# Kernel optimization log

Hardware: AMD Instinct MI355X
Metric: run time of the kernel (lower is better)

Reference implementation:

```python
import jax, jax.numpy as jnp
import numpy as np


def _lstm_dir(x, Wih, Whh, bih, bhh, reverse):
    """Single-direction LSTM. x: [T,B,Cin]; PyTorch gate order i,f,g,o."""
    T, B, _ = x.shape
    H = Whh.shape[1]
    # Precompute input-to-hidden GEMM for all timesteps at once: [T,B,4H]
    xg = jnp.einsum('tbc,gc->tbg', x, Wih) + (bih + bhh)

    def step(carry, xt):
        h, c = carry
        gates = xt + h @ Whh.T  # [B,4H]
        i, f, g, o = jnp.split(gates, 4, axis=-1)
        i = jax.nn.sigmoid(i)
        f = jax.nn.sigmoid(f)
        g = jnp.tanh(g)
        o = jax.nn.sigmoid(o)
        c = f * c + i * g
        h = o * jnp.tanh(c)
        return (h, c), h

    init = (jnp.zeros((B, H), x.dtype), jnp.zeros((B, H), x.dtype))
    _, hs = jax.lax.scan(step, init, xg, reverse=reverse)
    return hs  # [T,B,H], time-aligned with x for both directions


def _bilstm_layer(x, Wih_f, Whh_f, bih_f, bhh_f, Wih_b, Whh_b, bih_b, bhh_b):
    hf = _lstm_dir(x, Wih_f, Whh_f, bih_f, bhh_f, reverse=False)
    hb = _lstm_dir(x, Wih_b, Whh_b, bih_b, bhh_b, reverse=True)
    return jnp.concatenate([hf, hb], axis=-1)  # [T,B,2H]


def setup_inputs() -> dict:
    key = jax.random.key(0)
    ks = jax.random.split(key, 18)
    T, B, C, H = 160, 256, 512, 256
    G = 4 * H  # 1024
    s = 0.05  # small init to keep gates in the linear-ish regime
    inp = {"x": jax.random.normal(ks[0], (T, B, C), jnp.float32)}
    names = []
    for l, cin in ((0, C), (1, 2 * H)):
        for sfx in ("", "_reverse"):
            names.append((f"weight_ih_l{l}{sfx}", (G, cin)))
            names.append((f"weight_hh_l{l}{sfx}", (G, H)))
            names.append((f"bias_ih_l{l}{sfx}", (G,)))
            names.append((f"bias_hh_l{l}{sfx}", (G,)))
    for i, (nm, shp) in enumerate(names):
        inp[nm] = jax.random.normal(ks[i + 1], shp, jnp.float32) * s
    return inp


def reference(x,
              weight_ih_l0, weight_hh_l0, bias_ih_l0, bias_hh_l0,
              weight_ih_l0_reverse, weight_hh_l0_reverse, bias_ih_l0_reverse, bias_hh_l0_reverse,
              weight_ih_l1, weight_hh_l1, bias_ih_l1, bias_hh_l1,
              weight_ih_l1_reverse, weight_hh_l1_reverse, bias_ih_l1_reverse, bias_hh_l1_reverse):
    h0 = _bilstm_layer(x,
                       weight_ih_l0, weight_hh_l0, bias_ih_l0, bias_hh_l0,
                       weight_ih_l0_reverse, weight_hh_l0_reverse, bias_ih_l0_reverse, bias_hh_l0_reverse)
    h1 = _bilstm_layer(h0,
                       weight_ih_l1, weight_hh_l1, bias_ih_l1, bias_hh_l1,
                       weight_ih_l1_reverse, weight_hh_l1_reverse, bias_ih_l1_reverse, bias_hh_l1_reverse)
    return h1  # [T, B, 2H]
```

## Files before the change

kernel.cpp:

```cpp
#include <hip/hip_runtime.h>
#include <stdint.h>

typedef __attribute__((ext_vector_type(8))) short bf16x8;
typedef __attribute__((ext_vector_type(4))) float f32x4;

__device__ __forceinline__ float bf2f(unsigned short u) {
    union { unsigned int u32; float f; } v; v.u32 = ((unsigned int)u) << 16; return v.f;
}
__device__ __forceinline__ unsigned short f2bf(float f) {
    union { float f; unsigned int u32; } v; v.f = f;
    unsigned int r = v.u32 + 0x7FFFu + ((v.u32 >> 16) & 1u);
    return (unsigned short)(r >> 16);
}
__device__ __forceinline__ float sigm(float x) { return 1.f / (1.f + __expf(-x)); }
__device__ __forceinline__ float tanh_fast(float x) {
    float ax = fabsf(x);
    float e = __expf(-2.f * ax);
    float t = (1.f - e) / (1.f + e);
    return copysignf(t, x);
}

__global__ void f2bf_kernel(const float* __restrict__ src, unsigned short* __restrict__ dst, int n4) {
    int i = blockIdx.x * blockDim.x + threadIdx.x;
    if (i >= n4) return;
    float4 v = ((const float4*)src)[i];
    ushort4 o;
    o.x = f2bf(v.x); o.y = f2bf(v.y); o.z = f2bf(v.z); o.w = f2bf(v.w);
    ((ushort4*)dst)[i] = o;
}

__global__ void bias_comb_kernel(const float* __restrict__ bif, const float* __restrict__ bhf,
                                 const float* __restrict__ bir, const float* __restrict__ bhr,
                                 float* __restrict__ out) {
    int n = blockIdx.x * blockDim.x + threadIdx.x;
    if (n >= 2048) return;
    out[n] = (n < 1024) ? (bif[n] + bhf[n]) : (bir[n - 1024] + bhr[n - 1024]);
}

__global__ __launch_bounds__(256, 2) void gemm_bt_bias(
    const unsigned short* __restrict__ A, const unsigned short* __restrict__ B,
    const float* __restrict__ bias, unsigned short* __restrict__ C,
    int M, int N, int K) {
    const int bn0 = blockIdx.x * 128;
    const int bm0 = blockIdx.y * 128;
    const int tid = threadIdx.x;
    const int wave = tid >> 6, lane = tid & 63;
    const int ln15 = lane & 15, quad = lane >> 4;
    const int wr = wave >> 1, wc = wave & 1;

    __shared__ __align__(16) unsigned short At[128 * 72];
    __shared__ __align__(16) unsigned short Bt[128 * 72];

    f32x4 acc[4][4] = {};

    for (int ko = 0; ko < K; ko += 64) {
#pragma unroll
        for (int i = 0; i < 4; ++i) {
            int chunk = tid + i * 256;
            int row = chunk >> 3, cc = chunk & 7;
            *(bf16x8*)&At[row * 72 + cc * 8] = *(const bf16x8*)&A[(size_t)(bm0 + row) * K + ko + cc * 8];
            *(bf16x8*)&Bt[row * 72 + cc * 8] = *(const bf16x8*)&B[(size_t)(bn0 + row) * K + ko + cc * 8];
        }
        __syncthreads();
#pragma unroll
        for (int kk = 0; kk < 2; ++kk) {
            bf16x8 a[4], b[4];
#pragma unroll
            for (int f = 0; f < 4; ++f) {
                a[f] = *(const bf16x8*)&At[(wr * 64 + f * 16 + ln15) * 72 + kk * 32 + quad * 8];
                b[f] = *(const bf16x8*)&Bt[(wc * 64 + f * 16 + ln15) * 72 + kk * 32 + quad * 8];
            }
#pragma unroll
            for (int fi = 0; fi < 4; ++fi)
#pragma unroll
                for (int fj = 0; fj < 4; ++fj)
                    acc[fi][fj] = __builtin_amdgcn_mfma_f32_16x16x32_bf16(a[fi], b[fj], acc[fi][fj], 0, 0, 0);
        }
        __syncthreads();
    }
#pragma unroll
    for (int fi = 0; fi < 4; ++fi) {
        int row = bm0 + wr * 64 + fi * 16 + quad * 4;
#pragma unroll
        for (int fj = 0; fj < 4; ++fj) {
            int col = bn0 + wc * 64 + fj * 16 + ln15;
            float bv = bias[col];
#pragma unroll
            for (int r = 0; r < 4; ++r)
                C[(size_t)(row + r) * N + col] = f2bf(acc[fi][fj][r] + bv);
        }
    }
}

__global__ __launch_bounds__(256, 1) void lstm_scan4(
    const unsigned short* __restrict__ xg,
    const unsigned short* __restrict__ whh_f,
    const unsigned short* __restrict__ whh_r,
    unsigned short* __restrict__ out_bf,
    float* __restrict__ out_f,
    unsigned short* __restrict__ hexg)
{
    const int gid = blockIdx.x & 31;
    const int cg = blockIdx.x >> 5;
    const int dir = gid & 1, bg = gid >> 1;
    const int m0 = bg * 16;
    const int tid = threadIdx.x;
    const int wave = tid >> 6, lane = tid & 63;
    const int ln15 = lane & 15, quad = lane >> 4;
    const unsigned short* __restrict__ whh = dir ? whh_r : whh_f;

    __shared__ float gbuf[2][16 * 260];

    bf16x8 Bfr[32];
#pragma unroll
    for (int kb = 0; kb < 8; ++kb)
#pragma unroll
        for (int nt = 0; nt < 4; ++nt)
            Bfr[kb * 4 + nt] = *(const bf16x8*)&whh[
                (size_t)(wave * 256 + cg * 64 + nt * 16 + ln15) * 256 + kb * 32 + quad * 8];

    const int cm = tid >> 4, cj = tid & 15;
    float c[4] = {0.f, 0.f, 0.f, 0.f};

    unsigned long long* hex64 = (unsigned long long*)hexg;
    const unsigned long long SENT = ~0ull;

    for (int tt = 0; tt < 160; ++tt) {
        const int t = dir ? (159 - tt) : tt;

        f32x4 acc[4];
        {
            const unsigned short* xr = xg + (size_t)(t * 256 + m0 + quad * 4) * 2048
                                          + dir * 1024 + wave * 256 + cg * 64 + ln15;
#pragma unroll
            for (int nt = 0; nt < 4; ++nt)
#pragma unroll
                for (int r = 0; r < 4; ++r)
                    acc[nt][r] = bf2f(xr[(size_t)r * 2048 + nt * 16]);
        }

        const int slot_r = (tt + 7) & 7;
        unsigned long long* hsrc = hex64 + ((size_t)(slot_r * 2 + dir) * 16 + bg) * 1024
                                 + ln15 * 64 + quad * 2;
        unsigned long long w[16];
        {
            int lim = 1 << 20;
            for (;;) {
                bool ok = true;
#pragma unroll
                for (int kb = 0; kb < 8; ++kb) {
                    w[kb * 2]     = __hip_atomic_load(hsrc + kb * 8,     __ATOMIC_RELAXED, __HIP_MEMORY_SCOPE_AGENT);
                    w[kb * 2 + 1] = __hip_atomic_load(hsrc + kb * 8 + 1, __ATOMIC_RELAXED, __HIP_MEMORY_SCOPE_AGENT);
                }
#pragma unroll
                for (int i = 0; i < 16; ++i) ok &= (w[i] != SENT);
                if (ok || !--lim) break;
                __builtin_amdgcn_s_sleep(2);
            }
        }

        {
            const int slot_p = (tt + 6) & 7;
            unsigned long long* pp = hex64 + ((size_t)(slot_p * 2 + dir) * 16 + bg) * 1024
                                   + cm * 64 + cg * 16 + cj;
            __hip_atomic_store(pp, SENT, __ATOMIC_RELAXED, __HIP_MEMORY_SCOPE_AGENT);
        }

        bf16x8 af[8];
#pragma unroll
        for (int kb = 0; kb < 8; ++kb) {
            union { unsigned long long u[2]; bf16x8 v; } tm;
            tm.u[0] = w[kb * 2]; tm.u[1] = w[kb * 2 + 1];
            af[kb] = tm.v;
        }

#pragma unroll
        for (int kb = 0; kb < 8; ++kb)
#pragma unroll
            for (int nt = 0; nt < 4; ++nt)
                acc[nt] = __builtin_amdgcn_mfma_f32_16x16x32_bf16(af[kb], Bfr[kb * 4 + nt], acc[nt], 0, 0, 0);

        const int par = tt & 1;
#pragma unroll
        for (int nt = 0; nt < 4; ++nt)
#pragma unroll
            for (int r = 0; r < 4; ++r) {
                float v = acc[nt][r];
                v = (wave == 2) ? tanh_fast(v) : sigm(v);
                gbuf[par][(quad * 4 + r) * 260 + wave * 64 + nt * 16 + ln15] = v;
            }
        __syncthreads();

        const int slot_w = tt & 7;
        unsigned long long* hdst = hex64 + ((size_t)(slot_w * 2 + dir) * 16 + bg) * 1024;
        const float* gb = gbuf[par] + cm * 260;
        float hv[4];
#pragma unroll
        for (int p = 0; p < 4; ++p) {
            int lj = cj * 4 + p;
            float iv = gb[lj];
            float fv = gb[64 + lj];
            float gv = gb[128 + lj];
            float ov = gb[192 + lj];
            float cn = fv * c[p] + iv * gv;
            c[p] = cn;
            hv[p] = ov * tanh_fast(cn);
        }
        unsigned long long pk = (unsigned long long)f2bf(hv[0])
                              | ((unsigned long long)f2bf(hv[1]) << 16)
                              | ((unsigned long long)f2bf(hv[2]) << 32)
                              | ((unsigned long long)f2bf(hv[3]) << 48);
        __hip_atomic_store(hdst + cm * 64 + cg * 16 + cj, pk,
                           __ATOMIC_RELAXED, __HIP_MEMORY_SCOPE_AGENT);

        size_t obase = (size_t)(t * 256 + m0 + cm) * 512 + dir * 256 + cg * 64 + cj * 4;
        if (out_f) {
            float4 o4; o4.x = hv[0]; o4.y = hv[1]; o4.z = hv[2]; o4.w = hv[3];
            *(float4*)&out_f[obase] = o4;
        } else {
            ushort4 o4;
            o4.x = f2bf(hv[0]); o4.y = f2bf(hv[1]); o4.z = f2bf(hv[2]); o4.w = f2bf(hv[3]);
            *(ushort4*)&out_bf[obase] = o4;
        }
    }
}

extern "C" void kernel_launch(void* const* d_in, const int* in_sizes, int n_in,
                              void* d_out, int out_size, void* d_ws, size_t ws_size,
                              hipStream_t stream) {
    const float* x = (const float*)d_in[0];
    float* out = (float*)d_out;
    char* ws = (char*)d_ws;

    unsigned short* xbf   = (unsigned short*)(ws + 0);
    unsigned short* wcat0 = (unsigned short*)(ws + 41943040LL);
    unsigned short* wcat1 = (unsigned short*)(ws + 44040192LL);
    unsigned short* whh0f = (unsigned short*)(ws + 46137344LL);
    unsigned short* whh0r = whh0f + 262144;
    unsigned short* whh1f = whh0f + 524288;
    unsigned short* whh1r = whh0f + 786432;
    float* bias0          = (float*)(ws + 48234496LL);
    float* bias1          = (float*)(ws + 48242688LL);
    unsigned short* xgbuf = (unsigned short*)(ws + 48250880LL);
    unsigned short* hexg  = wcat0;
    unsigned short* h0b   = xbf;

    f2bf_kernel<<<20480, 256, 0, stream>>>(x, xbf, 5242880);
    f2bf_kernel<<<512, 256, 0, stream>>>((const float*)d_in[1], wcat0, 131072);
    f2bf_kernel<<<512, 256, 0, stream>>>((const float*)d_in[5], wcat0 + 524288, 131072);
    f2bf_kernel<<<512, 256, 0, stream>>>((const float*)d_in[9], wcat1, 131072);
    f2bf_kernel<<<512, 256, 0, stream>>>((const float*)d_in[13], wcat1 + 524288, 131072);
    f2bf_kernel<<<256, 256, 0, stream>>>((const float*)d_in[2], whh0f, 65536);
    f2bf_kernel<<<256, 256, 0, stream>>>((const float*)d_in[6], whh0r, 65536);
    f2bf_kernel<<<256, 256, 0, stream>>>((const float*)d_in[10], whh1f, 65536);
    f2bf_kernel<<<256, 256, 0, stream>>>((const float*)d_in[14], whh1r, 65536);
    bias_comb_kernel<<<8, 256, 0, stream>>>((const float*)d_in[3], (const float*)d_in[4],
                                            (const float*)d_in[7], (const float*)d_in[8], bias0);
    bias_comb_kernel<<<8, 256, 0, stream>>>((const float*)d_in[11], (const float*)d_in[12],
                                            (const float*)d_in[15], (const float*)d_in[16], bias1);

    dim3 gg(16, 320);
    gemm_bt_bias<<<gg, 256, 0, stream>>>(xbf, wcat0, bias0, xgbuf, 40960, 2048, 512);
    hipMemsetAsync(hexg, 0xFF, 2097152, stream);
    hipMemsetAsync((char*)hexg + 7 * 262144, 0, 262144, stream);
    lstm_scan4<<<128, 256, 0, stream>>>(xgbuf, whh0f, whh0r, h0b, nullptr, hexg);
    gemm_bt_bias<<<gg, 256, 0, stream>>>(h0b, wcat1, bias1, xgbuf, 40960, 2048, 512);
    hipMemsetAsync(hexg, 0xFF, 2097152, stream);
    hipMemsetAsync((char*)hexg + 7 * 262144, 0, 262144, stream);
    lstm_scan4<<<128, 256, 0, stream>>>(xgbuf, whh1f, whh1r, nullptr, out, hexg);
}
```

Measured before the change: 1.743 ms.

## Restructure LSTM scan: per-wave gate ownership, sc0 polling, x prefetch

Reorganizes the recurrent scan so each wave computes all four gates for its own hidden columns. This removes the LDS gate buffer and one of the two block barriers per timestep. The next timestep's input-gate values are prefetched into registers, and lane shuffles repack h into the exchange layout. A startup handshake checks whether plain sc0 loads and stores are coherent across the blocks. If they are, inline-asm dwordx4 polling without sleep replaces the agent-scope atomics, otherwise the atomic path is kept. The non-atomic path depends on cache-coherence behaviour, and the handshake adds startup overhead.

```diff
diff --git a/kernel.cpp b/kernel.cpp
--- a/kernel.cpp
+++ b/kernel.cpp
@@ -3,6 +3,7 @@
 
 typedef __attribute__((ext_vector_type(8))) short bf16x8;
 typedef __attribute__((ext_vector_type(4))) float f32x4;
+typedef __attribute__((ext_vector_type(2))) unsigned long long u64x2;
 
 __device__ __forceinline__ float bf2f(unsigned short u) {
     union { unsigned int u32; float f; } v; v.u32 = ((unsigned int)u) << 16; return v.f;
@@ -92,137 +93,240 @@
     }
 }
 
-__global__ __launch_bounds__(256, 1) void lstm_scan4(
+__device__ __forceinline__ void st1_sc0(unsigned long long* p, unsigned long long v) {
+    asm volatile("global_store_dwordx2 %0, %1, off sc0" :: "v"(p), "v"(v) : "memory");
+}
+__device__ __forceinline__ unsigned long long ld1_sc0(const unsigned long long* p) {
+    unsigned long long v;
+    asm volatile("global_load_dwordx2 %0, %1, off sc0\n\ts_waitcnt vmcnt(0)"
+                 : "=v"(v) : "v"(p) : "memory");
+    return v;
+}
+
+template<bool FAST>
+__device__ void scan_loop(const unsigned short* __restrict__ xg,
+                          const unsigned short* __restrict__ whh,
+                          unsigned short* __restrict__ out_bf,
+                          float* __restrict__ out_f,
+                          unsigned long long* hex64, int dir, int bg, int cg)
+{
+    const int tid = threadIdx.x;
+    const int wave = tid >> 6, lane = tid & 63;
+    const int ln15 = lane & 15, quad = lane >> 4;
+    const int m0 = bg * 16;
+    const int rowr = quad * 4 + (ln15 & 3);
+    const int colg = cg * 16 + wave * 4 + (ln15 >> 2);
+    const unsigned long long SENT = ~0ull;
+    const unsigned long long M16 = 0x0000FFFF0000FFFFull;
+
+    bf16x8 Bfr[32];
+#pragma unroll
+    for (int kb = 0; kb < 8; ++kb)
+#pragma unroll
+        for (int g = 0; g < 4; ++g)
+            Bfr[kb * 4 + g] = *(const bf16x8*)&whh[
+                (size_t)(g * 256 + cg * 64 + wave * 16 + ln15) * 256 + kb * 32 + quad * 8];
+
+    float c[4] = {0.f, 0.f, 0.f, 0.f};
+    const unsigned short* xbase = xg + (size_t)(m0 + quad * 4) * 2048
+                                     + dir * 1024 + cg * 64 + wave * 16 + ln15;
+
+    unsigned short xvA[16], xvB[16];
+    {
+        const int t0 = dir ? 159 : 0;
+        const unsigned short* xr = xbase + (size_t)t0 * 256 * 2048;
+#pragma unroll
+        for (int g = 0; g < 4; ++g)
+#pragma unroll
+            for (int r = 0; r < 4; ++r)
+                xvA[g * 4 + r] = xr[(size_t)r * 2048 + g * 256];
+    }
+
+    auto step = [&](int tt, unsigned short (&xu)[16], unsigned short (&xp)[16]) {
+        const int t = dir ? (159 - tt) : tt;
+
+        const int slot_r = (tt + 7) & 7;
+        unsigned long long* hsrc = hex64 + ((size_t)(slot_r * 2 + dir) * 16 + bg) * 1024
+                                 + ln15 * 64 + quad * 2;
+        unsigned long long w[16];
+        if (FAST) {
+            u64x2 wv[8];
+            int lim = 1 << 16;
+            for (;;) {
+#define RL(I, OFF) asm volatile("global_load_dwordx4 %0, %1, off offset:" OFF " sc0" : "=v"(wv[I]) : "v"(hsrc))
+                RL(0, "0");  RL(1, "64");  RL(2, "128"); RL(3, "192");
+                RL(4, "256"); RL(5, "320"); RL(6, "384"); RL(7, "448");
+#undef RL
+                asm volatile("s_waitcnt vmcnt(0)" ::: "memory");
+                __builtin_amdgcn_sched_barrier(0);
+                bool ok = true;
+#pragma unroll
+                for (int i = 0; i < 8; ++i) ok &= (wv[i][0] != SENT) & (wv[i][1] != SENT);
+                if (ok || !--lim) break;
+            }
+#pragma unroll
+            for (int i = 0; i < 8; ++i) { w[i * 2] = wv[i][0]; w[i * 2 + 1] = wv[i][1]; }
+        } else {
+            int lim = 1 << 17;
+            for (;;) {
+#pragma unroll
+                for (int kb = 0; kb < 8; ++kb) {
+                    w[kb * 2]     = __hip_atomic_load(hsrc + kb * 8,     __ATOMIC_RELAXED, __HIP_MEMORY_SCOPE_AGENT);
+                    w[kb * 2 + 1] = __hip_atomic_load(hsrc + kb * 8 + 1, __ATOMIC_RELAXED, __HIP_MEMORY_SCOPE_AGENT);
+                }
+                bool ok = true;
+#pragma unroll
+                for (int i = 0; i < 16; ++i) ok &= (w[i] != SENT);
+                if (ok || !--lim) break;
+                __builtin_amdgcn_s_sleep(2);
+            }
+        }
+
+        __syncthreads();
+
+        {
+            const int ttn = (tt < 159) ? tt + 1 : tt;
+            const int tn = dir ? (159 - ttn) : ttn;
+            const unsigned short* xr = xbase + (size_t)tn * 256 * 2048;
+#pragma unroll
+            for (int g = 0; g < 4; ++g)
+#pragma unroll
+                for (int r = 0; r < 4; ++r)
+                    xp[g * 4 + r] = xr[(size_t)r * 2048 + g * 256];
+        }
+
+        bf16x8 af[8];
+#pragma unroll
+        for (int kb = 0; kb < 8; ++kb) {
+            union { unsigned long long u[2]; bf16x8 v; } tm;
+            tm.u[0] = w[kb * 2]; tm.u[1] = w[kb * 2 + 1];
+            af[kb] = tm.v;
+        }
+        f32x4 acc[4] = {};
+#pragma unroll
+        for (int kb = 0; kb < 8; ++kb)
+#pragma unroll
+            for (int g = 0; g < 4; ++g)
+                acc[g] = __builtin_amdgcn_mfma_f32_16x16x32_bf16(af[kb], Bfr[kb * 4 + g], acc[g], 0, 0, 0);
+
+        float hv[4];
+#pragma unroll
+        for (int r = 0; r < 4; ++r) {
+            float iv = sigm(acc[0][r] + bf2f(xu[0 + r]));
+            float fv = sigm(acc[1][r] + bf2f(xu[4 + r]));
+            float gv = tanh_fast(acc[2][r] + bf2f(xu[8 + r]));
+            float ov = sigm(acc[3][r] + bf2f(xu[12 + r]));
+            float cn = fv * c[r] + iv * gv;
+            c[r] = cn;
+            hv[r] = ov * tanh_fast(cn);
+        }
+
+        unsigned long long P = (unsigned long long)f2bf(hv[0])
+                             | ((unsigned long long)f2bf(hv[1]) << 16)
+                             | ((unsigned long long)f2bf(hv[2]) << 32)
+                             | ((unsigned long long)f2bf(hv[3]) << 48);
+        unsigned long long X = __shfl_xor(P, 2);
+        unsigned long long Nn = (ln15 & 2) ? ((X >> 32) | (P & 0xFFFFFFFF00000000ull))
+                                           : ((P & 0x00000000FFFFFFFFull) | (X << 32));
+        unsigned long long Y = __shfl_xor(Nn, 1);
+        unsigned long long Q = (ln15 & 1) ? (((Y >> 16) & M16) | (((Nn >> 16) & M16) << 16))
+                                          : ((Nn & M16) | ((Y & M16) << 16));
+
+        unsigned long long* hdst = hex64 + ((size_t)((tt & 7) * 2 + dir) * 16 + bg) * 1024
+                                 + rowr * 64 + colg;
+        if (FAST) st1_sc0(hdst, Q);
+        else __hip_atomic_store(hdst, Q, __ATOMIC_RELAXED, __HIP_MEMORY_SCOPE_AGENT);
+
+        {
+            const int slot_p = (tt + 6) & 7;
+            unsigned long long* pp = hex64 + ((size_t)(slot_p * 2 + dir) * 16 + bg) * 1024
+                                   + rowr * 64 + colg;
+            if (FAST) st1_sc0(pp, SENT);
+            else __hip_atomic_store(pp, SENT, __ATOMIC_RELAXED, __HIP_MEMORY_SCOPE_AGENT);
+        }
+
+        if (out_f) {
+            size_t ob = (size_t)(t * 256 + m0 + quad * 4) * 512 + dir * 256
+                      + cg * 64 + wave * 16 + ln15;
+#pragma unroll
+            for (int r = 0; r < 4; ++r) out_f[ob + (size_t)r * 512] = hv[r];
+        } else {
+            size_t ob = (size_t)(t * 256 + m0 + rowr) * 512 + dir * 256
+                      + cg * 64 + wave * 16 + (ln15 >> 2) * 4;
+            *(unsigned long long*)&out_bf[ob] = Q;
+        }
+    };
+
+    for (int tt = 0; tt < 160; tt += 2) { step(tt, xvA, xvB); step(tt + 1, xvB, xvA); }
+}
+
+__global__ __launch_bounds__(256, 1) void lstm_scan7(
     const unsigned short* __restrict__ xg,
     const unsigned short* __restrict__ whh_f,
     const unsigned short* __restrict__ whh_r,
     unsigned short* __restrict__ out_bf,
     float* __restrict__ out_f,
-    unsigned short* __restrict__ hexg)
+    unsigned short* __restrict__ hexg,
+    unsigned long long* __restrict__ sync)
 {
     const int gid = blockIdx.x & 31;
     const int cg = blockIdx.x >> 5;
     const int dir = gid & 1, bg = gid >> 1;
-    const int m0 = bg * 16;
-    const int tid = threadIdx.x;
-    const int wave = tid >> 6, lane = tid & 63;
-    const int ln15 = lane & 15, quad = lane >> 4;
     const unsigned short* __restrict__ whh = dir ? whh_r : whh_f;
-
-    __shared__ float gbuf[2][16 * 260];
-
-    bf16x8 Bfr[32];
-#pragma unroll
-    for (int kb = 0; kb < 8; ++kb)
-#pragma unroll
-        for (int nt = 0; nt < 4; ++nt)
-            Bfr[kb * 4 + nt] = *(const bf16x8*)&whh[
-                (size_t)(wave * 256 + cg * 64 + nt * 16 + ln15) * 256 + kb * 32 + quad * 8];
-
-    const int cm = tid >> 4, cj = tid & 15;
-    float c[4] = {0.f, 0.f, 0.f, 0.f};
-
     unsigned long long* hex64 = (unsigned long long*)hexg;
-    const unsigned long long SENT = ~0ull;
-
-    for (int tt = 0; tt < 160; ++tt) {
-        const int t = dir ? (159 - tt) : tt;
-
-        f32x4 acc[4];
-        {
-            const unsigned short* xr = xg + (size_t)(t * 256 + m0 + quad * 4) * 2048
-                                          + dir * 1024 + wave * 256 + cg * 64 + ln15;
-#pragma unroll
-            for (int nt = 0; nt < 4; ++nt)
-#pragma unroll
-                for (int r = 0; r < 4; ++r)
-                    acc[nt][r] = bf2f(xr[(size_t)r * 2048 + nt * 16]);
-        }
-
-        const int slot_r = (tt + 7) & 7;
-        unsigned long long* hsrc = hex64 + ((size_t)(slot_r * 2 + dir) * 16 + bg) * 1024
-                                 + ln15 * 64 + quad * 2;
-        unsigned long long w[16];
+
+    __shared__ int s_fast;
+    if (threadIdx.x == 0) {
+        unsigned long long* can = sync;
+        int* SA = (int*)(sync + 128);
+        int* RR = SA + 128;
+        const int b = blockIdx.x;
+        const unsigned long long M1 = 0x1111111111111111ull, M2 = 0x2222222222222222ull;
+        int ok = 1;
+        st1_sc0(&can[b], M1);
+        {
+            int lim = 1 << 14;
+            for (int p = 0; p < 4; ++p) {
+                unsigned long long v;
+                do { v = ld1_sc0(&can[gid + 32 * p]); } while (v != M1 && --lim > 0);
+                if (v != M1) ok = 0;
+            }
+        }
+        __hip_atomic_store(&SA[b], 1, __ATOMIC_RELAXED, __HIP_MEMORY_SCOPE_AGENT);
         {
             int lim = 1 << 20;
-            for (;;) {
-                bool ok = true;
-#pragma unroll
-                for (int kb = 0; kb < 8; ++kb) {
-                    w[kb * 2]     = __hip_atomic_load(hsrc + kb * 8,     __ATOMIC_RELAXED, __HIP_MEMORY_SCOPE_AGENT);
-                    w[kb * 2 + 1] = __hip_atomic_load(hsrc + kb * 8 + 1, __ATOMIC_RELAXED, __HIP_MEMORY_SCOPE_AGENT);
-                }
-#pragma unroll
-                for (int i = 0; i < 16; ++i) ok &= (w[i] != SENT);
-                if (ok || !--lim) break;
-                __builtin_amdgcn_s_sleep(2);
-            }
-        }
-
-        {
-            const int slot_p = (tt + 6) & 7;
-            unsigned long long* pp = hex64 + ((size_t)(slot_p * 2 + dir) * 16 + bg) * 1024
-                                   + cm * 64 + cg * 16 + cj;
-            __hip_atomic_store(pp, SENT, __ATOMIC_RELAXED, __HIP_MEMORY_SCOPE_AGENT);
-        }
-
-        bf16x8 af[8];
-#pragma unroll
-        for (int kb = 0; kb < 8; ++kb) {
-            union { unsigned long long u[2]; bf16x8 v; } tm;
-            tm.u[0] = w[kb * 2]; tm.u[1] = w[kb * 2 + 1];
-            af[kb] = tm.v;
-        }
-
-#pragma unroll
-        for (int kb = 0; kb < 8; ++kb)
-#pragma unroll
-            for (int nt = 0; nt < 4; ++nt)
-                acc[nt] = __builtin_amdgcn_mfma_f32_16x16x32_bf16(af[kb], Bfr[kb * 4 + nt], acc[nt], 0, 0, 0);
-
-        const int par = tt & 1;
-#pragma unroll
-        for (int nt = 0; nt < 4; ++nt)
-#pragma unroll
-            for (int r = 0; r < 4; ++r) {
-                float v = acc[nt][r];
-                v = (wave == 2) ? tanh_fast(v) : sigm(v);
-                gbuf[par][(quad * 4 + r) * 260 + wave * 64 + nt * 16 + ln15] = v;
-            }
-        __syncthreads();
-
-        const int slot_w = tt & 7;
-        unsigned long long* hdst = hex64 + ((size_t)(slot_w * 2 + dir) * 16 + bg) * 1024;
-        const float* gb = gbuf[par] + cm * 260;
-        float hv[4];
-#pragma unroll
-        for (int p = 0; p < 4; ++p) {
-            int lj = cj * 4 + p;
-            float iv = gb[lj];
-            float fv = gb[64 + lj];
-            float gv = gb[128 + lj];
-            float ov = gb[192 + lj];
-            float cn = fv * c[p] + iv * gv;
-            c[p] = cn;
-            hv[p] = ov * tanh_fast(cn);
-        }
-        unsigned long long pk = (unsigned long long)f2bf(hv[0])
-                              | ((unsigned long long)f2bf(hv[1]) << 16)
-                              | ((unsigned long long)f2bf(hv[2]) << 32)
-                              | ((unsigned long long)f2bf(hv[3]) << 48);
-        __hip_atomic_store(hdst + cm * 64 + cg * 16 + cj, pk,
-                           __ATOMIC_RELAXED, __HIP_MEMORY_SCOPE_AGENT);
-
-        size_t obase = (size_t)(t * 256 + m0 + cm) * 512 + dir * 256 + cg * 64 + cj * 4;
-        if (out_f) {
-            float4 o4; o4.x = hv[0]; o4.y = hv[1]; o4.z = hv[2]; o4.w = hv[3];
-            *(float4*)&out_f[obase] = o4;
-        } else {
-            ushort4 o4;
-            o4.x = f2bf(hv[0]); o4.y = f2bf(hv[1]); o4.z = f2bf(hv[2]); o4.w = f2bf(hv[3]);
-            *(ushort4*)&out_bf[obase] = o4;
-        }
+            for (int p = 0; p < 4; ++p) {
+                int v;
+                do { v = __hip_atomic_load(&SA[gid + 32 * p], __ATOMIC_RELAXED, __HIP_MEMORY_SCOPE_AGENT); }
+                while (v != 1 && --lim > 0);
+                if (v != 1) ok = 0;
+            }
+        }
+        st1_sc0(&can[b], M2);
+        {
+            int lim = 1 << 14;
+            for (int p = 0; p < 4; ++p) {
+                unsigned long long v;
+                do { v = ld1_sc0(&can[gid + 32 * p]); } while (v != M2 && --lim > 0);
+                if (v != M2) ok = 0;
+            }
+        }
+        __hip_atomic_store(&RR[b], ok, __ATOMIC_RELAXED, __HIP_MEMORY_SCOPE_AGENT);
+        int fast = 1;
+        {
+            int lim = 1 << 20;
+            for (int p = 0; p < 4; ++p) {
+                int v;
+                do { v = __hip_atomic_load(&RR[gid + 32 * p], __ATOMIC_RELAXED, __HIP_MEMORY_SCOPE_AGENT); }
+                while (v == -1 && --lim > 0);
+                fast &= (v == 1);
+            }
+        }
+        s_fast = fast;
     }
+    __syncthreads();
+    if (s_fast) scan_loop<true>(xg, whh, out_bf, out_f, hex64, dir, bg, cg);
+    else        scan_loop<false>(xg, whh, out_bf, out_f, hex64, dir, bg, cg);
 }
 
 extern "C" void kernel_launch(void* const* d_in, const int* in_sizes, int n_in,
@@ -242,6 +346,7 @@
     float* bias0          = (float*)(ws + 48234496LL);
     float* bias1          = (float*)(ws + 48242688LL);
     unsigned short* xgbuf = (unsigned short*)(ws + 48250880LL);
+    unsigned long long* syncb = (unsigned long long*)(ws + 216023040LL);
     unsigned short* hexg  = wcat0;
     unsigned short* h0b   = xbf;
 
@@ -263,9 +368,11 @@
     gemm_bt_bias<<<gg, 256, 0, stream>>>(xbf, wcat0, bias0, xgbuf, 40960, 2048, 512);
     hipMemsetAsync(hexg, 0xFF, 2097152, stream);
     hipMemsetAsync((char*)hexg + 7 * 262144, 0, 262144, stream);
-    lstm_scan4<<<128, 256, 0, stream>>>(xgbuf, whh0f, whh0r, h0b, nullptr, hexg);
+    hipMemsetAsync(syncb, 0xFF, 2048, stream);
+    lstm_scan7<<<128, 256, 0, stream>>>(xgbuf, whh0f, whh0r, h0b, nullptr, hexg, syncb);
     gemm_bt_bias<<<gg, 256, 0, stream>>>(h0b, wcat1, bias1, xgbuf, 40960, 2048, 512);
     hipMemsetAsync(hexg, 0xFF, 2097152, stream);
     hipMemsetAsync((char*)hexg + 7 * 262144, 0, 262144, stream);
-    lstm_scan4<<<128, 256, 0, stream>>>(xgbuf, whh1f, whh1r, nullptr, out, hexg);
-}
+    hipMemsetAsync(syncb, 0xFF, 2048, stream);
+    lstm_scan7<<<128, 256, 0, stream>>>(xgbuf, whh1f, whh1r, nullptr, out, hexg, syncb);
+}
```

Result: slower. 5.392 ms (+209.3%).

## Restructure LSTM scan with per-block flags, in-register gates, and x prefetch

Applied to the files above, without the earlier changes.

Replaces the per-element sentinel polling on the hidden-state exchange buffer with per-timestep block flags that one thread spins on, followed by a block barrier. Remaps the recurrent weights so each wave holds all four gates for its columns, so the gate nonlinearities and cell update run in registers without the shared-memory gate buffer. Packs h with lane shuffles, double-buffers h in two slots instead of eight, and prefetches next-step xg values. Adds an extra __syncthreads per step plus a flag store/poll, and relies on relaxed atomics for ordering between the h stores and the flag.

```diff
diff --git a/kernel.cpp b/kernel.cpp
--- a/kernel.cpp
+++ b/kernel.cpp
@@ -92,13 +92,14 @@
     }
 }
 
-__global__ __launch_bounds__(256, 1) void lstm_scan4(
+__global__ __launch_bounds__(256, 1) void lstm_scan8(
     const unsigned short* __restrict__ xg,
     const unsigned short* __restrict__ whh_f,
     const unsigned short* __restrict__ whh_r,
     unsigned short* __restrict__ out_bf,
     float* __restrict__ out_f,
-    unsigned short* __restrict__ hexg)
+    unsigned short* __restrict__ hexg,
+    int* __restrict__ flags)
 {
     const int gid = blockIdx.x & 31;
     const int cg = blockIdx.x >> 5;
@@ -107,63 +108,73 @@
     const int tid = threadIdx.x;
     const int wave = tid >> 6, lane = tid & 63;
     const int ln15 = lane & 15, quad = lane >> 4;
+    const int rowr = quad * 4 + (ln15 & 3);
+    const int colg = cg * 16 + wave * 4 + (ln15 >> 2);
     const unsigned short* __restrict__ whh = dir ? whh_r : whh_f;
-
-    __shared__ float gbuf[2][16 * 260];
+    const unsigned long long M16 = 0x0000FFFF0000FFFFull;
+    unsigned long long* hex64 = (unsigned long long*)hexg;
+    int* fgrp = flags + gid * 160 * 4;
 
     bf16x8 Bfr[32];
 #pragma unroll
     for (int kb = 0; kb < 8; ++kb)
 #pragma unroll
-        for (int nt = 0; nt < 4; ++nt)
-            Bfr[kb * 4 + nt] = *(const bf16x8*)&whh[
-                (size_t)(wave * 256 + cg * 64 + nt * 16 + ln15) * 256 + kb * 32 + quad * 8];
-
-    const int cm = tid >> 4, cj = tid & 15;
+        for (int g = 0; g < 4; ++g)
+            Bfr[kb * 4 + g] = *(const bf16x8*)&whh[
+                (size_t)(g * 256 + cg * 64 + wave * 16 + ln15) * 256 + kb * 32 + quad * 8];
+
     float c[4] = {0.f, 0.f, 0.f, 0.f};
-
-    unsigned long long* hex64 = (unsigned long long*)hexg;
-    const unsigned long long SENT = ~0ull;
-
-    for (int tt = 0; tt < 160; ++tt) {
+    const unsigned short* xbase = xg + (size_t)(m0 + quad * 4) * 2048
+                                     + dir * 1024 + cg * 64 + wave * 16 + ln15;
+
+    unsigned short xvA[16], xvB[16];
+    {
+        const int t0 = dir ? 159 : 0;
+        const unsigned short* xr = xbase + (size_t)t0 * 256 * 2048;
+#pragma unroll
+        for (int g = 0; g < 4; ++g)
+#pragma unroll
+            for (int r = 0; r < 4; ++r)
+                xvA[g * 4 + r] = xr[(size_t)r * 2048 + g * 256];
+    }
+
+    auto step = [&](int tt, unsigned short (&xu)[16], unsigned short (&xp)[16]) {
         const int t = dir ? (159 - tt) : tt;
 
-        f32x4 acc[4];
-        {
-            const unsigned short* xr = xg + (size_t)(t * 256 + m0 + quad * 4) * 2048
-                                          + dir * 1024 + wave * 256 + cg * 64 + ln15;
-#pragma unroll
-            for (int nt = 0; nt < 4; ++nt)
-#pragma unroll
-                for (int r = 0; r < 4; ++r)
-                    acc[nt][r] = bf2f(xr[(size_t)r * 2048 + nt * 16]);
-        }
-
-        const int slot_r = (tt + 7) & 7;
+        if (tt > 0) {
+            if (tid == 0) {
+                const int* fp = fgrp + (tt - 1) * 4;
+                int lim = 1 << 22;
+                for (;;) {
+                    int a0 = __hip_atomic_load(fp + 0, __ATOMIC_RELAXED, __HIP_MEMORY_SCOPE_AGENT);
+                    int a1 = __hip_atomic_load(fp + 1, __ATOMIC_RELAXED, __HIP_MEMORY_SCOPE_AGENT);
+                    int a2 = __hip_atomic_load(fp + 2, __ATOMIC_RELAXED, __HIP_MEMORY_SCOPE_AGENT);
+                    int a3 = __hip_atomic_load(fp + 3, __ATOMIC_RELAXED, __HIP_MEMORY_SCOPE_AGENT);
+                    if ((a0 & a1 & a2 & a3) || !--lim) break;
+                }
+            }
+            __syncthreads();
+        }
+
+        const int slot_r = (tt + 1) & 1;
         unsigned long long* hsrc = hex64 + ((size_t)(slot_r * 2 + dir) * 16 + bg) * 1024
                                  + ln15 * 64 + quad * 2;
         unsigned long long w[16];
+#pragma unroll
+        for (int kb = 0; kb < 8; ++kb) {
+            w[kb * 2]     = __hip_atomic_load(hsrc + kb * 8,     __ATOMIC_RELAXED, __HIP_MEMORY_SCOPE_AGENT);
+            w[kb * 2 + 1] = __hip_atomic_load(hsrc + kb * 8 + 1, __ATOMIC_RELAXED, __HIP_MEMORY_SCOPE_AGENT);
+        }
+
         {
-            int lim = 1 << 20;
-            for (;;) {
-                bool ok = true;
-#pragma unroll
-                for (int kb = 0; kb < 8; ++kb) {
-                    w[kb * 2]     = __hip_atomic_load(hsrc + kb * 8,     __ATOMIC_RELAXED, __HIP_MEMORY_SCOPE_AGENT);
-                    w[kb * 2 + 1] = __hip_atomic_load(hsrc + kb * 8 + 1, __ATOMIC_RELAXED, __HIP_MEMORY_SCOPE_AGENT);
-                }
-#pragma unroll
-                for (int i = 0; i < 16; ++i) ok &= (w[i] != SENT);
-                if (ok || !--lim) break;
-                __builtin_amdgcn_s_sleep(2);
-            }
-        }
-
-        {
-            const int slot_p = (tt + 6) & 7;
-            unsigned long long* pp = hex64 + ((size_t)(slot_p * 2 + dir) * 16 + bg) * 1024
-                                   + cm * 64 + cg * 16 + cj;
-            __hip_atomic_store(pp, SENT, __ATOMIC_RELAXED, __HIP_MEMORY_SCOPE_AGENT);
+            const int ttn = (tt < 159) ? tt + 1 : tt;
+            const int tn = dir ? (159 - ttn) : ttn;
+            const unsigned short* xr = xbase + (size_t)tn * 256 * 2048;
+#pragma unroll
+            for (int g = 0; g < 4; ++g)
+#pragma unroll
+                for (int r = 0; r < 4; ++r)
+                    xp[g * 4 + r] = xr[(size_t)r * 2048 + g * 256];
         }
 
         bf16x8 af[8];
@@ -173,56 +184,57 @@
             tm.u[0] = w[kb * 2]; tm.u[1] = w[kb * 2 + 1];
             af[kb] = tm.v;
         }
-
+        f32x4 acc[4] = {};
 #pragma unroll
         for (int kb = 0; kb < 8; ++kb)
 #pragma unroll
-            for (int nt = 0; nt < 4; ++nt)
-                acc[nt] = __builtin_amdgcn_mfma_f32_16x16x32_bf16(af[kb], Bfr[kb * 4 + nt], acc[nt], 0, 0, 0);
-
-        const int par = tt & 1;
-#pragma unroll
-        for (int nt = 0; nt < 4; ++nt)
-#pragma unroll
-            for (int r = 0; r < 4; ++r) {
-                float v = acc[nt][r];
-                v = (wave == 2) ? tanh_fast(v) : sigm(v);
-                gbuf[par][(quad * 4 + r) * 260 + wave * 64 + nt * 16 + ln15] = v;
-            }
+            for (int g = 0; g < 4; ++g)
+                acc[g] = __builtin_amdgcn_mfma_f32_16x16x32_bf16(af[kb], Bfr[kb * 4 + g], acc[g], 0, 0, 0);
+
+        float hv[4];
+#pragma unroll
+        for (int r = 0; r < 4; ++r) {
+            float iv = sigm(acc[0][r] + bf2f(xu[0 + r]));
+            float fv = sigm(acc[1][r] + bf2f(xu[4 + r]));
+            float gv = tanh_fast(acc[2][r] + bf2f(xu[8 + r]));
+            float ov = sigm(acc[3][r] + bf2f(xu[12 + r]));
+            float cn = fv * c[r] + iv * gv;
+            c[r] = cn;
+            hv[r] = ov * tanh_fast(cn);
+        }
+
+        unsigned long long P = (unsigned long long)f2bf(hv[0])
+                             | ((unsigned long long)f2bf(hv[1]) << 16)
+                             | ((unsigned long long)f2bf(hv[2]) << 32)
+                             | ((unsigned long long)f2bf(hv[3]) << 48);
+        unsigned long long X = __shfl_xor(P, 2);
+        unsigned long long Nn = (ln15 & 2) ? ((X >> 32) | (P & 0xFFFFFFFF00000000ull))
+                                           : ((P & 0x00000000FFFFFFFFull) | (X << 32));
+        unsigned long long Y = __shfl_xor(Nn, 1);
+        unsigned long long Q = (ln15 & 1) ? (((Y >> 16) & M16) | (((Nn >> 16) & M16) << 16))
+                                          : ((Nn & M16) | ((Y & M16) << 16));
+
+        unsigned long long* hdst = hex64 + ((size_t)((tt & 1) * 2 + dir) * 16 + bg) * 1024
+                                 + rowr * 64 + colg;
+        __hip_atomic_store(hdst, Q, __ATOMIC_RELAXED, __HIP_MEMORY_SCOPE_AGENT);
+
         __syncthreads();
-
-        const int slot_w = tt & 7;
-        unsigned long long* hdst = hex64 + ((size_t)(slot_w * 2 + dir) * 16 + bg) * 1024;
-        const float* gb = gbuf[par] + cm * 260;
-        float hv[4];
-#pragma unroll
-        for (int p = 0; p < 4; ++p) {
-            int lj = cj * 4 + p;
-            float iv = gb[lj];
-            float fv = gb[64 + lj];
-            float gv = gb[128 + lj];
-            float ov = gb[192 + lj];
-            float cn = fv * c[p] + iv * gv;
-            c[p] = cn;
-            hv[p] = ov * tanh_fast(cn);
-        }
-        unsigned long long pk = (unsigned long long)f2bf(hv[0])
-                              | ((unsigned long long)f2bf(hv[1]) << 16)
-                              | ((unsigned long long)f2bf(hv[2]) << 32)
-                              | ((unsigned long long)f2bf(hv[3]) << 48);
-        __hip_atomic_store(hdst + cm * 64 + cg * 16 + cj, pk,
-                           __ATOMIC_RELAXED, __HIP_MEMORY_SCOPE_AGENT);
-
-        size_t obase = (size_t)(t * 256 + m0 + cm) * 512 + dir * 256 + cg * 64 + cj * 4;
+        if (tid == 0)
+            __hip_atomic_store(fgrp + tt * 4 + cg, 1, __ATOMIC_RELAXED, __HIP_MEMORY_SCOPE_AGENT);
+
         if (out_f) {
-            float4 o4; o4.x = hv[0]; o4.y = hv[1]; o4.z = hv[2]; o4.w = hv[3];
-            *(float4*)&out_f[obase] = o4;
+            size_t ob = (size_t)(t * 256 + m0 + quad * 4) * 512 + dir * 256
+                      + cg * 64 + wave * 16 + ln15;
+#pragma unroll
+            for (int r = 0; r < 4; ++r) out_f[ob + (size_t)r * 512] = hv[r];
         } else {
-            ushort4 o4;
-            o4.x = f2bf(hv[0]); o4.y = f2bf(hv[1]); o4.z = f2bf(hv[2]); o4.w = f2bf(hv[3]);
-            *(ushort4*)&out_bf[obase] = o4;
-        }
-    }
+            size_t ob = (size_t)(t * 256 + m0 + rowr) * 512 + dir * 256
+                      + cg * 64 + wave * 16 + (ln15 >> 2) * 4;
+            *(unsigned long long*)&out_bf[ob] = Q;
+        }
+    };
+
+    for (int tt = 0; tt < 160; tt += 2) { step(tt, xvA, xvB); step(tt + 1, xvB, xvA); }
 }
 
 extern "C" void kernel_launch(void* const* d_in, const int* in_sizes, int n_in,
@@ -242,6 +254,7 @@
     float* bias0          = (float*)(ws + 48234496LL);
     float* bias1          = (float*)(ws + 48242688LL);
     unsigned short* xgbuf = (unsigned short*)(ws + 48250880LL);
+    int* flagbuf          = (int*)(ws + 216023040LL);
     unsigned short* hexg  = wcat0;
     unsigned short* h0b   = xbf;
 
@@ -261,11 +274,11 @@
 
     dim3 gg(16, 320);
     gemm_bt_bias<<<gg, 256, 0, stream>>>(xbf, wcat0, bias0, xgbuf, 40960, 2048, 512);
-    hipMemsetAsync(hexg, 0xFF, 2097152, stream);
-    hipMemsetAsync((char*)hexg + 7 * 262144, 0, 262144, stream);
-    lstm_scan4<<<128, 256, 0, stream>>>(xgbuf, whh0f, whh0r, h0b, nullptr, hexg);
+    hipMemsetAsync(hexg, 0, 524288, stream);
+    hipMemsetAsync(flagbuf, 0, 81920, stream);
+    lstm_scan8<<<128, 256, 0, stream>>>(xgbuf, whh0f, whh0r, h0b, nullptr, hexg, flagbuf);
     gemm_bt_bias<<<gg, 256, 0, stream>>>(h0b, wcat1, bias1, xgbuf, 40960, 2048, 512);
-    hipMemsetAsync(hexg, 0xFF, 2097152, stream);
-    hipMemsetAsync((char*)hexg + 7 * 262144, 0, 262144, stream);
-    lstm_scan4<<<128, 256, 0, stream>>>(xgbuf, whh1f, whh1r, nullptr, out, hexg);
-}
+    hipMemsetAsync(hexg, 0, 524288, stream);
+    hipMemsetAsync(flagbuf, 0, 81920, stream);
+    lstm_scan8<<<128, 256, 0, stream>>>(xgbuf, whh1f, whh1r, nullptr, out, hexg, flagbuf);
+}
```

After: 1.530 ms. 1.14x faster.
